# Kernel tuning notes

Measured on AMD Instinct MI355X. Metric: run time of the kernel, lower is better.

The kernel has to match this reference:

```python
import jax, jax.numpy as jnp
import numpy as np
from jax import lax

B, T, D, H = 64, 512, 512, 512


def setup_inputs() -> dict:
    key = jax.random.key(0)
    k1, k2 = jax.random.split(key)
    x = jax.random.normal(k1, (B, T, D), dtype=jnp.float32)
    # single fused gate weight: concat([h, x]) -> 4 gates of size H (f, i, o, c_bar)
    W = jax.random.normal(k2, (H + D, 4 * H), dtype=jnp.float32) * (1.0 / np.sqrt(H + D))
    b = jnp.zeros((4 * H,), dtype=jnp.float32)
    return {"x": x, "W": W, "b": b}


def reference(x, W, b):
    """LSTM per source math: c' = sig(f)*c + sig(i)*c_bar ; h' = sig(o)*c' (no tanh)."""
    Bb = x.shape[0]
    Hh = W.shape[1] // 4
    dt = x.dtype

    def step(carry, xt):
        h, c = carry
        z = jnp.concatenate([h, xt], axis=-1) @ W + b  # [B, 4H]
        f, i, o, c_bar = jnp.split(z, 4, axis=-1)
        c_new = jax.nn.sigmoid(f) * c + jax.nn.sigmoid(i) * c_bar
        h_new = jax.nn.sigmoid(o) * c_new
        return (h_new, c_new), h_new

    init = (jnp.zeros((Bb, Hh), dt), jnp.zeros((Bb, Hh), dt))
    _, hs = lax.scan(step, init, jnp.swapaxes(x, 0, 1))  # hs: [T, B, H]
    return jnp.swapaxes(hs, 0, 1)  # [B, T, H]
```

## Files before the change

### kernel.cpp

```cpp
#include <hip/hip_runtime.h>
#include <math.h>

#define Bz 64
#define Tz 512
#define Dz 512
#define Hz 512

#define WB_FLOATS   (64*1024*32)
#define HBUF_FLOATS (64*512)

__global__ __launch_bounds__(256) void zero_ws(float* __restrict__ p, int n) {
    int i = blockIdx.x * 256 + threadIdx.x;
    if (i < n) p[i] = 0.0f;
}

__global__ __launch_bounds__(256) void prep_w(const float* __restrict__ W,
                                              float* __restrict__ Wb) {
    int k = blockIdx.x;
    for (int it = 0; it < 8; ++it) {
        int col = it * 256 + threadIdx.x;
        float v = W[(size_t)k * 2048 + col];
        int g = col >> 9, rem = col & 511;
        int cg = rem >> 3, hc = rem & 7;
        int c = g * 8 + hc;
        Wb[((size_t)cg * 1024 + k) * 32 + c] = v;
    }
}

__global__ __launch_bounds__(256) void lstm_step(
    const float* __restrict__ x,
    const float* __restrict__ bias,
    const float* __restrict__ Wb,
    const float* __restrict__ hbr,
    float* __restrict__ hbw,
    float* __restrict__ cbuf,
    float* __restrict__ out,
    int t)
{
    const int cg  = blockIdx.x;
    const int sg  = blockIdx.y;
    const int tid = threadIdx.x;

    __shared__ float As[16 * 1028];
    __shared__ float zpart[8 * 512];
    __shared__ float zred[512];

    for (int it = 0; it < 16; ++it) {
        int fi = it * 256 + tid;
        int s  = fi >> 8;
        int k  = (fi & 255) * 4;
        const float* src;
        if (k < 512) src = hbr + (sg * 16 + s) * 512 + k;
        else         src = x + (size_t)(sg * 16 + s) * Tz * Dz
                             + (size_t)t * Dz + (k - 512);
        float4 v = *(const float4*)src;
        *(float4*)(As + s * 1028 + k) = v;
    }
    __syncthreads();

    const int ct = tid & 7;
    const int st = (tid >> 3) & 3;
    const int kw = tid >> 5;

    float acc[4][4];
#pragma unroll
    for (int i = 0; i < 4; ++i)
#pragma unroll
        for (int j = 0; j < 4; ++j) acc[i][j] = 0.0f;

    const float* wp = Wb + (size_t)cg * 1024 * 32 + (size_t)(kw * 128) * 32 + ct * 4;
    const float* ap = As + st * 4 * 1028 + kw * 128;

#pragma unroll 4
    for (int kk = 0; kk < 128; kk += 4) {
        float4 w0 = *(const float4*)(wp + (kk + 0) * 32);
        float4 w1 = *(const float4*)(wp + (kk + 1) * 32);
        float4 w2 = *(const float4*)(wp + (kk + 2) * 32);
        float4 w3 = *(const float4*)(wp + (kk + 3) * 32);
        float4 a0 = *(const float4*)(ap + 0 * 1028 + kk);
        float4 a1 = *(const float4*)(ap + 1 * 1028 + kk);
        float4 a2 = *(const float4*)(ap + 2 * 1028 + kk);
        float4 a3 = *(const float4*)(ap + 3 * 1028 + kk);
#define FMA_ROW(i, ai)                                              \
        acc[i][0] += ai.x * w0.x + ai.y * w1.x + ai.z * w2.x + ai.w * w3.x; \
        acc[i][1] += ai.x * w0.y + ai.y * w1.y + ai.z * w2.y + ai.w * w3.y; \
        acc[i][2] += ai.x * w0.z + ai.y * w1.z + ai.z * w2.z + ai.w * w3.z; \
        acc[i][3] += ai.x * w0.w + ai.y * w1.w + ai.z * w2.w + ai.w * w3.w;
        FMA_ROW(0, a0)
        FMA_ROW(1, a1)
        FMA_ROW(2, a2)
        FMA_ROW(3, a3)
#undef FMA_ROW
    }

#pragma unroll
    for (int i = 0; i < 4; ++i) {
        float4 v = make_float4(acc[i][0], acc[i][1], acc[i][2], acc[i][3]);
        *(float4*)(zpart + kw * 512 + (st * 4 + i) * 32 + ct * 4) = v;
    }
    __syncthreads();

    {
        int o = tid * 2;
        float z0 = 0.0f, z1 = 0.0f;
#pragma unroll
        for (int w = 0; w < 8; ++w) {
            float2 v = *(const float2*)(zpart + w * 512 + o);
            z0 += v.x; z1 += v.y;
        }
        *(float2*)(zred + o) = make_float2(z0, z1);
    }
    __syncthreads();

    if (tid < 128) {
        int s  = tid >> 3;
        int hc = tid & 7;
        int colb = cg * 8 + hc;
        float zf = zred[s * 32 + hc]       + bias[colb];
        float zi = zred[s * 32 + 8 + hc]   + bias[512 + colb];
        float zo = zred[s * 32 + 16 + hc]  + bias[1024 + colb];
        float zc = zred[s * 32 + 24 + hc]  + bias[1536 + colb];

        int cidx = (sg * 64 + cg) * 128 + tid;
        float cold = cbuf[cidx];
        float sf = 1.0f / (1.0f + expf(-zf));
        float si = 1.0f / (1.0f + expf(-zi));
        float so = 1.0f / (1.0f + expf(-zo));
        float cnew = sf * cold + si * zc;
        float h = so * cnew;
        cbuf[cidx] = cnew;

        hbw[(sg * 16 + s) * 512 + colb] = h;
        out[(size_t)(sg * 16 + s) * Tz * Hz + (size_t)t * Hz + colb] = h;
    }
}

extern "C" void kernel_launch(void* const* d_in, const int* in_sizes, int n_in,
                              void* d_out, int out_size, void* d_ws, size_t ws_size,
                              hipStream_t stream) {
    const float* x    = (const float*)d_in[0];
    const float* W    = (const float*)d_in[1];
    const float* bias = (const float*)d_in[2];
    float* out = (float*)d_out;

    char* ws = (char*)d_ws;
    float* Wb   = (float*)ws;
    float* hbuf = (float*)(ws + (size_t)WB_FLOATS * 4);
    float* cbuf = hbuf + 2 * HBUF_FLOATS;

    zero_ws<<<384, 256, 0, stream>>>(hbuf, 98304);
    prep_w<<<1024, 256, 0, stream>>>(W, Wb);

    for (int t = 0; t < Tz; ++t) {
        float* hr = hbuf + (t & 1) * HBUF_FLOATS;
        float* hw = hbuf + ((t + 1) & 1) * HBUF_FLOATS;
        lstm_step<<<dim3(64, 4), 256, 0, stream>>>(x, bias, Wb, hr, hw, cbuf, out, t);
    }
}
```

Measured before the change: 7.778 ms.

## Replace per-timestep launches with persistent kernel using grid barrier and LDS-resident weights

Swaps the 512 per-timestep kernel launches for a single persistent kernel of 256 blocks that loops over time and synchronises through a global atomic counter barrier. Each block keeps its 128KB weight slice in LDS and its cell state in registers, and streams the h/x activations through a double-buffered LDS chunk pipeline. This removes launch overhead and the repeated weight reads from global memory. In exchange it relies on all 256 blocks being co-resident, which a grid-wide spin barrier requires and the launch bounds (256,1) with large LDS use are meant to allow, and it adds extra barriers per chunk.

Measured after the change: 23.94 ms. +207.8%, slower.

```diff
diff --git a/kernel.cpp b/kernel.cpp
--- a/kernel.cpp
+++ b/kernel.cpp
@@ -1,13 +1,10 @@
 #include <hip/hip_runtime.h>
 #include <math.h>
 
-#define Bz 64
-#define Tz 512
-#define Dz 512
-#define Hz 512
-
+
+#define APAD 132
+#define HBUF_FLOATS (64*512)
 #define WB_FLOATS   (64*1024*32)
-#define HBUF_FLOATS (64*512)
 
 __global__ __launch_bounds__(256) void zero_ws(float* __restrict__ p, int n) {
     int i = blockIdx.x * 256 + threadIdx.x;
@@ -22,116 +19,165 @@
         float v = W[(size_t)k * 2048 + col];
         int g = col >> 9, rem = col & 511;
         int cg = rem >> 3, hc = rem & 7;
-        int c = g * 8 + hc;
-        Wb[((size_t)cg * 1024 + k) * 32 + c] = v;
-    }
-}
-
-__global__ __launch_bounds__(256) void lstm_step(
+        Wb[((size_t)cg * 1024 + k) * 32 + g * 8 + hc] = v;
+    }
+}
+
+__global__ __launch_bounds__(256, 1) void lstm_persist(
     const float* __restrict__ x,
     const float* __restrict__ bias,
     const float* __restrict__ Wb,
-    const float* __restrict__ hbr,
-    float* __restrict__ hbw,
-    float* __restrict__ cbuf,
-    float* __restrict__ out,
-    int t)
+    float* __restrict__ hbuf,
+    unsigned* __restrict__ bar,
+    float* __restrict__ out)
 {
-    const int cg  = blockIdx.x;
-    const int sg  = blockIdx.y;
+    __shared__ float Ws[32768];
+    __shared__ float As[2][16 * APAD];
+    __shared__ float zred[512];
+    float* const zpart = &As[0][0];
+
     const int tid = threadIdx.x;
-
-    __shared__ float As[16 * 1028];
-    __shared__ float zpart[8 * 512];
-    __shared__ float zred[512];
-
-    for (int it = 0; it < 16; ++it) {
-        int fi = it * 256 + tid;
-        int s  = fi >> 8;
-        int k  = (fi & 255) * 4;
-        const float* src;
-        if (k < 512) src = hbr + (sg * 16 + s) * 512 + k;
-        else         src = x + (size_t)(sg * 16 + s) * Tz * Dz
-                             + (size_t)t * Dz + (k - 512);
-        float4 v = *(const float4*)src;
-        *(float4*)(As + s * 1028 + k) = v;
-    }
-    __syncthreads();
+    const int cg  = blockIdx.x & 63;
+    const int sg  = blockIdx.x >> 6;
+
+    {
+        const float* wsrc = Wb + (size_t)cg * 32768;
+        for (int i = 0; i < 32; ++i) {
+            int fi = (i * 256 + tid) * 4;
+            *(float4*)(Ws + fi) = *(const float4*)(wsrc + fi);
+        }
+    }
 
     const int ct = tid & 7;
     const int st = (tid >> 3) & 3;
     const int kw = tid >> 5;
 
-    float acc[4][4];
-#pragma unroll
-    for (int i = 0; i < 4; ++i)
-#pragma unroll
-        for (int j = 0; j < 4; ++j) acc[i][j] = 0.0f;
-
-    const float* wp = Wb + (size_t)cg * 1024 * 32 + (size_t)(kw * 128) * 32 + ct * 4;
-    const float* ap = As + st * 4 * 1028 + kw * 128;
-
-#pragma unroll 4
-    for (int kk = 0; kk < 128; kk += 4) {
-        float4 w0 = *(const float4*)(wp + (kk + 0) * 32);
-        float4 w1 = *(const float4*)(wp + (kk + 1) * 32);
-        float4 w2 = *(const float4*)(wp + (kk + 2) * 32);
-        float4 w3 = *(const float4*)(wp + (kk + 3) * 32);
-        float4 a0 = *(const float4*)(ap + 0 * 1028 + kk);
-        float4 a1 = *(const float4*)(ap + 1 * 1028 + kk);
-        float4 a2 = *(const float4*)(ap + 2 * 1028 + kk);
-        float4 a3 = *(const float4*)(ap + 3 * 1028 + kk);
-#define FMA_ROW(i, ai)                                              \
-        acc[i][0] += ai.x * w0.x + ai.y * w1.x + ai.z * w2.x + ai.w * w3.x; \
-        acc[i][1] += ai.x * w0.y + ai.y * w1.y + ai.z * w2.y + ai.w * w3.y; \
-        acc[i][2] += ai.x * w0.z + ai.y * w1.z + ai.z * w2.z + ai.w * w3.z; \
-        acc[i][3] += ai.x * w0.w + ai.y * w1.w + ai.z * w2.w + ai.w * w3.w;
-        FMA_ROW(0, a0)
-        FMA_ROW(1, a1)
-        FMA_ROW(2, a2)
-        FMA_ROW(3, a3)
+    const int s0  = tid >> 5;
+    const int f40 = tid & 31;
+
+    const int es = tid >> 3, ehc = tid & 7;
+    float bf = 0, bi = 0, bo = 0, bc = 0;
+    if (tid < 128) {
+        int colb = cg * 8 + ehc;
+        bf = bias[colb];
+        bi = bias[512 + colb];
+        bo = bias[1024 + colb];
+        bc = bias[1536 + colb];
+    }
+    float creg = 0.0f;
+
+    __syncthreads();
+
+    unsigned target = 0;
+    for (int t = 0; t < 512; ++t) {
+        const float* hr = hbuf + (t & 1) * HBUF_FLOATS;
+        float*       hw = hbuf + ((t + 1) & 1) * HBUF_FLOATS;
+
+        float acc[4][4];
+#pragma unroll
+        for (int i = 0; i < 4; ++i)
+#pragma unroll
+            for (int j = 0; j < 4; ++j) acc[i][j] = 0.0f;
+
+        {
+            float4 v0 = *(const float4*)(hr + (sg * 16 + s0) * 512 + f40 * 4);
+            float4 v1 = *(const float4*)(hr + (sg * 16 + s0 + 8) * 512 + f40 * 4);
+            *(float4*)(&As[0][s0 * APAD + f40 * 4]) = v0;
+            *(float4*)(&As[0][(s0 + 8) * APAD + f40 * 4]) = v1;
+        }
+        __syncthreads();
+
+        for (int ch = 0; ch < 8; ++ch) {
+            float4 p0, p1;
+            if (ch < 7) {
+                int kb = (ch + 1) * 128 + f40 * 4;
+                const float *src0, *src1;
+                if (kb < 512) {
+                    src0 = hr + (sg * 16 + s0) * 512 + kb;
+                    src1 = hr + (sg * 16 + s0 + 8) * 512 + kb;
+                } else {
+                    src0 = x + ((size_t)(sg * 16 + s0) * 512 + t) * 512 + (kb - 512);
+                    src1 = x + ((size_t)(sg * 16 + s0 + 8) * 512 + t) * 512 + (kb - 512);
+                }
+                p0 = *(const float4*)src0;
+                p1 = *(const float4*)src1;
+            }
+
+            const float* ap = &As[ch & 1][st * 4 * APAD + kw * 16];
+            const float* wp = Ws + (ch * 128 + kw * 16) * 32 + ct * 4;
+#pragma unroll
+            for (int kk = 0; kk < 16; kk += 4) {
+                float4 w0 = *(const float4*)(wp + (kk + 0) * 32);
+                float4 w1 = *(const float4*)(wp + (kk + 1) * 32);
+                float4 w2 = *(const float4*)(wp + (kk + 2) * 32);
+                float4 w3 = *(const float4*)(wp + (kk + 3) * 32);
+                float4 a0 = *(const float4*)(ap + 0 * APAD + kk);
+                float4 a1 = *(const float4*)(ap + 1 * APAD + kk);
+                float4 a2 = *(const float4*)(ap + 2 * APAD + kk);
+                float4 a3 = *(const float4*)(ap + 3 * APAD + kk);
+#define FMA_ROW(i, ai)                                                      \
+                acc[i][0] += ai.x * w0.x + ai.y * w1.x + ai.z * w2.x + ai.w * w3.x; \
+                acc[i][1] += ai.x * w0.y + ai.y * w1.y + ai.z * w2.y + ai.w * w3.y; \
+                acc[i][2] += ai.x * w0.z + ai.y * w1.z + ai.z * w2.z + ai.w * w3.z; \
+                acc[i][3] += ai.x * w0.w + ai.y * w1.w + ai.z * w2.w + ai.w * w3.w;
+                FMA_ROW(0, a0)
+                FMA_ROW(1, a1)
+                FMA_ROW(2, a2)
+                FMA_ROW(3, a3)
 #undef FMA_ROW
-    }
-
-#pragma unroll
-    for (int i = 0; i < 4; ++i) {
-        float4 v = make_float4(acc[i][0], acc[i][1], acc[i][2], acc[i][3]);
-        *(float4*)(zpart + kw * 512 + (st * 4 + i) * 32 + ct * 4) = v;
-    }
-    __syncthreads();
-
-    {
-        int o = tid * 2;
-        float z0 = 0.0f, z1 = 0.0f;
-#pragma unroll
-        for (int w = 0; w < 8; ++w) {
-            float2 v = *(const float2*)(zpart + w * 512 + o);
-            z0 += v.x; z1 += v.y;
-        }
-        *(float2*)(zred + o) = make_float2(z0, z1);
-    }
-    __syncthreads();
-
-    if (tid < 128) {
-        int s  = tid >> 3;
-        int hc = tid & 7;
-        int colb = cg * 8 + hc;
-        float zf = zred[s * 32 + hc]       + bias[colb];
-        float zi = zred[s * 32 + 8 + hc]   + bias[512 + colb];
-        float zo = zred[s * 32 + 16 + hc]  + bias[1024 + colb];
-        float zc = zred[s * 32 + 24 + hc]  + bias[1536 + colb];
-
-        int cidx = (sg * 64 + cg) * 128 + tid;
-        float cold = cbuf[cidx];
-        float sf = 1.0f / (1.0f + expf(-zf));
-        float si = 1.0f / (1.0f + expf(-zi));
-        float so = 1.0f / (1.0f + expf(-zo));
-        float cnew = sf * cold + si * zc;
-        float h = so * cnew;
-        cbuf[cidx] = cnew;
-
-        hbw[(sg * 16 + s) * 512 + colb] = h;
-        out[(size_t)(sg * 16 + s) * Tz * Hz + (size_t)t * Hz + colb] = h;
+            }
+
+            if (ch < 7) {
+                float* dst = &As[(ch + 1) & 1][0];
+                *(float4*)(dst + s0 * APAD + f40 * 4) = p0;
+                *(float4*)(dst + (s0 + 8) * APAD + f40 * 4) = p1;
+            }
+            __syncthreads();
+        }
+
+#pragma unroll
+        for (int i = 0; i < 4; ++i) {
+            *(float4*)(zpart + kw * 512 + (st * 4 + i) * 32 + ct * 4) =
+                make_float4(acc[i][0], acc[i][1], acc[i][2], acc[i][3]);
+        }
+        __syncthreads();
+        {
+            int o = tid * 2;
+            float z0 = 0.0f, z1 = 0.0f;
+#pragma unroll
+            for (int w = 0; w < 8; ++w) {
+                float2 v = *(const float2*)(zpart + w * 512 + o);
+                z0 += v.x; z1 += v.y;
+            }
+            *(float2*)(zred + o) = make_float2(z0, z1);
+        }
+        __syncthreads();
+
+        if (tid < 128) {
+            float zf = zred[es * 32 + ehc]      + bf;
+            float zi = zred[es * 32 + 8 + ehc]  + bi;
+            float zo = zred[es * 32 + 16 + ehc] + bo;
+            float zc = zred[es * 32 + 24 + ehc] + bc;
+            float sf = 1.0f / (1.0f + expf(-zf));
+            float si = 1.0f / (1.0f + expf(-zi));
+            float so = 1.0f / (1.0f + expf(-zo));
+            creg = sf * creg + si * zc;
+            float h = so * creg;
+            int colb = cg * 8 + ehc;
+            hw[(sg * 16 + es) * 512 + colb] = h;
+            out[((size_t)(sg * 16 + es) * 512 + t) * 512 + colb] = h;
+        }
+
+        target += 256;
+        __threadfence();
+        __syncthreads();
+        if (tid == 0) {
+            __hip_atomic_fetch_add(bar, 1u, __ATOMIC_RELEASE, __HIP_MEMORY_SCOPE_AGENT);
+            while (__hip_atomic_load(bar, __ATOMIC_ACQUIRE, __HIP_MEMORY_SCOPE_AGENT) < target)
+                __builtin_amdgcn_s_sleep(1);
+            __threadfence();
+        }
+        __syncthreads();
     }
 }
 
@@ -144,16 +190,11 @@
     float* out = (float*)d_out;
 
     char* ws = (char*)d_ws;
-    float* Wb   = (float*)ws;
-    float* hbuf = (float*)(ws + (size_t)WB_FLOATS * 4);
-    float* cbuf = hbuf + 2 * HBUF_FLOATS;
-
-    zero_ws<<<384, 256, 0, stream>>>(hbuf, 98304);
+    float* Wb       = (float*)ws;
+    float* hbuf     = (float*)(ws + (size_t)WB_FLOATS * 4);
+    unsigned* bar   = (unsigned*)(hbuf + 2 * HBUF_FLOATS);
+
+    zero_ws<<<257, 256, 0, stream>>>(hbuf, 2 * HBUF_FLOATS + 256);
     prep_w<<<1024, 256, 0, stream>>>(W, Wb);
-
-    for (int t = 0; t < Tz; ++t) {
-        float* hr = hbuf + (t & 1) * HBUF_FLOATS;
-        float* hw = hbuf + ((t + 1) & 1) * HBUF_FLOATS;
-        lstm_step<<<dim3(64, 4), 256, 0, stream>>>(x, bias, Wb, hr, hw, cbuf, out, t);
-    }
-}
+    lstm_persist<<<256, 256, 0, stream>>>(x, bias, Wb, hbuf, bar, out);
+}
```
